# Kernel tuning notes

Hardware: AMD Instinct MI355X
Metric: run time of the kernel (lower is better)

## Reference

```python
import jax, jax.numpy as jnp
import numpy as np

N = 100000
E = 1600000
F_IN = 128
H = 128


def setup_inputs() -> dict:
    key = jax.random.key(0)
    ks = jax.random.split(key, 12)
    x = jax.random.normal(ks[0], (N, F_IN), dtype=jnp.float32)
    edge_index = jax.random.randint(ks[1], (2, E), 0, N, dtype=jnp.int64)
    s = 1.0 / np.sqrt(F_IN)
    sh = 1.0 / np.sqrt(H)
    inp = {"x": x, "edge_index": edge_index}
    # SAGEConv params: lin_l (neighbor agg, with bias), lin_r (root, no bias)
    inp["W1l"] = jax.random.uniform(ks[2], (H, F_IN), jnp.float32, -s, s)
    inp["b1"] = jnp.zeros((H,), jnp.float32)
    inp["W1r"] = jax.random.uniform(ks[3], (H, F_IN), jnp.float32, -s, s)
    inp["W2l"] = jax.random.uniform(ks[4], (H, H), jnp.float32, -sh, sh)
    inp["b2"] = jnp.zeros((H,), jnp.float32)
    inp["W2r"] = jax.random.uniform(ks[5], (H, H), jnp.float32, -sh, sh)
    inp["W3l"] = jax.random.uniform(ks[6], (H, H), jnp.float32, -sh, sh)
    inp["b3"] = jnp.zeros((H,), jnp.float32)
    inp["W3r"] = jax.random.uniform(ks[7], (H, H), jnp.float32, -sh, sh)
    inp["Wo"] = jax.random.uniform(ks[8], (1, H), jnp.float32, -sh, sh)
    inp["bo"] = jnp.zeros((1,), jnp.float32)
    return inp


def _sage_max(h, src, dst, Wl, bl, Wr):
    # max-aggregate source features at destination nodes (empty -> 0, as PyG)
    m = jax.ops.segment_max(h[src], dst, num_segments=N)  # [N, d]
    m = jnp.where(jnp.isfinite(m), m, jnp.zeros_like(m))
    return m @ Wl.T + bl + h @ Wr.T


def reference(x, edge_index, W1l, b1, W1r, W2l, b2, W2r, W3l, b3, W3r, Wo, bo):
    src, dst = edge_index[0], edge_index[1]
    h1 = jax.nn.elu(_sage_max(x, src, dst, W1l, b1, W1r))
    h2 = jax.nn.elu(_sage_max(h1, src, dst, W2l, b2, W2r)) + h1
    h3 = jax.nn.elu(_sage_max(h2, src, dst, W3l, b3, W3r)) + h2
    return jax.nn.sigmoid(h3 @ Wo.T + bo)  # [N, 1]
```

## Files before the change

kernel.cpp:

```cpp
#include <hip/hip_runtime.h>
#include <hip/hip_fp16.h>
#include <math.h>

#define HDIM 128

#define BSHIFT 7
#define BW 128
#define BCAP 4096
#define NBKMAX 1024
#define CHUNK 4096

typedef __attribute__((ext_vector_type(8))) _Float16 f16x8;
typedef __attribute__((ext_vector_type(2))) _Float16 f16x2;
typedef __attribute__((ext_vector_type(16))) float f32x16;
typedef unsigned int uint32;
typedef unsigned short u16;

__device__ __forceinline__ uint32 hmax2u(uint32 a, uint32 b) {
    f16x2 ha = __builtin_bit_cast(f16x2, a);
    f16x2 hb = __builtin_bit_cast(f16x2, b);
    f16x2 r = __builtin_elementwise_max(ha, hb);
    return __builtin_bit_cast(uint32, r);
}
__device__ __forceinline__ uint32 hadd2u(uint32 a, uint32 b) {
    f16x2 ha = __builtin_bit_cast(f16x2, a);
    f16x2 hb = __builtin_bit_cast(f16x2, b);
    f16x2 r = ha + hb;
    return __builtin_bit_cast(uint32, r);
}


__global__ __launch_bounds__(256) void bucket_bin(
    const int* __restrict__ ei, int E_, int nbk,
    int* __restrict__ bucketCnt, uint32* __restrict__ tmp)
{
    __shared__ int cnt[NBKMAX];
    __shared__ int gbase[NBKMAX];
    const int t = threadIdx.x;
    const int start = blockIdx.x * CHUNK;
    const int end = min(start + CHUNK, E_);

    for (int i = t; i < nbk; i += 256) cnt[i] = 0;
    __syncthreads();
    for (int e = start + t; e < end; e += 256)
        atomicAdd(&cnt[ei[E_ + e] >> BSHIFT], 1);
    __syncthreads();
    for (int i = t; i < nbk; i += 256) {
        int c = cnt[i];
        gbase[i] = c ? atomicAdd(&bucketCnt[i], c) : 0;
    }
    __syncthreads();
    for (int i = t; i < nbk; i += 256) cnt[i] = 0;
    __syncthreads();
    for (int e = start + t; e < end; e += 256) {
        int d = ei[E_ + e];
        int s = ei[e];
        int b = d >> BSHIFT;
        int r = atomicAdd(&cnt[b], 1);
        tmp[(size_t)b * BCAP + gbase[b] + r] =
            ((uint32)(d & (BW - 1)) << 17) | (uint32)s;
    }
}

__global__ __launch_bounds__(1024) void bucket_scan(
    const int* __restrict__ bucketCnt, int* __restrict__ bucketBase,
    int nbk, int* __restrict__ off, int N_, int E_) {
    __shared__ int sd[1024];
    int t = threadIdx.x;
    int v = (t < nbk) ? bucketCnt[t] : 0;
    sd[t] = v;
    __syncthreads();
    for (int ofs = 1; ofs < 1024; ofs <<= 1) {
        int add = (t >= ofs) ? sd[t - ofs] : 0;
        __syncthreads();
        sd[t] += add;
        __syncthreads();
    }
    if (t < nbk) bucketBase[t] = sd[t] - v;
    if (t == 0) off[N_] = E_;
}

__global__ __launch_bounds__(256) void bucket_csr(
    const uint32* __restrict__ tmp, const int* __restrict__ bucketCnt,
    const int* __restrict__ bucketBase,
    int* __restrict__ off, int* __restrict__ srcs, int N_)
{
    __shared__ int lc[BW];
    __shared__ int lo[BW];
    __shared__ int sd[256];
    const int b = blockIdx.x, t = threadIdx.x;
    const int cnt = bucketCnt[b], base = bucketBase[b];
    const uint32* tp = tmp + (size_t)b * BCAP;

    if (t < BW) lc[t] = 0;
    __syncthreads();
    for (int i = t; i < cnt; i += 256) atomicAdd(&lc[tp[i] >> 17], 1);
    __syncthreads();

    int v = (t < BW) ? lc[t] : 0;
    sd[t] = v;
    __syncthreads();
    for (int ofs = 1; ofs < 256; ofs <<= 1) {
        int add = (t >= ofs) ? sd[t - ofs] : 0;
        __syncthreads();
        sd[t] += add;
        __syncthreads();
    }
    if (t < BW) lo[t] = sd[t] - v;
    __syncthreads();

    for (int i = t; i < BW; i += 256) {
        int node = b * BW + i;
        if (node < N_) off[node] = base + lo[i];
    }
    if (t < BW) lc[t] = lo[t];
    __syncthreads();
    for (int i = t; i < cnt; i += 256) {
        uint32 p = tp[i];
        int dl = p >> 17, s = p & 0x1FFFF;
        int pos = base + atomicAdd(&lc[dl], 1);
        srcs[pos] = s;
    }
}


__global__ void cast_x(const float* __restrict__ x, uint32* __restrict__ xb, int n2) {
    int i = blockIdx.x * 256 + threadIdx.x;
    if (i >= n2) return;
    float2 v = ((const float2*)x)[i];
    f16x2 h = { (_Float16)v.x, (_Float16)v.y };
    xb[i] = __builtin_bit_cast(uint32, h);
}

__global__ void cast_weights_packed(
    const float* __restrict__ W1l, const float* __restrict__ W1r,
    const float* __restrict__ W2l, const float* __restrict__ W2r,
    const float* __restrict__ W3l, const float* __restrict__ W3r,
    f16x8* __restrict__ PW)
{
    int tid = blockIdx.x * 256 + threadIdx.x;
    if (tid >= 3 * 4096) return;
    int layer = tid >> 12, rem = tid & 4095;
    int g = rem >> 10, ks = (rem >> 6) & 15, lane = rem & 63;
    int col = g * 32 + (lane & 31), kq = lane >> 5;
    const float* src;
    if (layer == 0)      src = (ks < 8) ? W1l : W1r;
    else if (layer == 1) src = (ks < 8) ? W2l : W2r;
    else                 src = (ks < 8) ? W3l : W3r;
    int kk = (ks & 7) * 16 + kq * 8;
    f16x8 v;
#pragma unroll
    for (int j = 0; j < 8; ++j) v[j] = (_Float16)src[col * HDIM + kk + j];
    PW[tid] = v;
}


#define ESTRIDE 136
#define EDGE_CAP 832

#define RED16(m0,m1,m2,m3,V) do { \
    m0 = hmax2u(m0, (V)[0].x); m1 = hmax2u(m1, (V)[0].y); \
    m2 = hmax2u(m2, (V)[0].z); m3 = hmax2u(m3, (V)[0].w); \
    m0 = hmax2u(m0, (V)[1].x); m1 = hmax2u(m1, (V)[1].y); \
    m2 = hmax2u(m2, (V)[1].z); m3 = hmax2u(m3, (V)[1].w); \
    m0 = hmax2u(m0, (V)[2].x); m1 = hmax2u(m1, (V)[2].y); \
    m2 = hmax2u(m2, (V)[2].z); m3 = hmax2u(m3, (V)[2].w); \
    m0 = hmax2u(m0, (V)[3].x); m1 = hmax2u(m1, (V)[3].y); \
    m2 = hmax2u(m2, (V)[3].z); m3 = hmax2u(m3, (V)[3].w); \
} while (0)

template<bool L>
__device__ __forceinline__ void issue_batch(
    const uint4* __restrict__ hp, const int* __restrict__ srcs,
    const int* sedge, int estart, int eb, int e1, int es, int ch, uint4* v)
{
    int last = e1 - 1;
#pragma unroll
    for (int k = 0; k < 4; ++k) {
        int idx = min(eb + es + 4 * k, last);
        int s = L ? sedge[idx - estart] : srcs[idx];
        v[k] = hp[(size_t)s * 16 + ch];
    }
}

template<bool L>
__device__ __forceinline__ void gather8(
    const uint4* __restrict__ hp, const int* __restrict__ srcs,
    const int* sedge, int estart, int offv, int es, int ch, int w,
    uint4* sm)
{
    const uint32 NINF = 0xFC00FC00u;
    uint4 vb[2][4];

    int e0 = __shfl(offv, 0), e1 = __shfl(offv, 1);
    bool has = e1 > e0;
    if (has) issue_batch<L>(hp, srcs, sedge, estart, e0, e1, es, ch, vb[0]);

#pragma unroll
    for (int i = 0; i < 8; ++i) {
        int e0n = 0, e1n = 0; bool hasn = false;
        if (i + 1 < 8) {
            e0n = __shfl(offv, i + 1); e1n = __shfl(offv, i + 2);
            hasn = e1n > e0n;
            if (hasn) issue_batch<L>(hp, srcs, sedge, estart, e0n, e1n, es, ch, vb[(i + 1) & 1]);
        }
        uint32 m0 = NINF, m1 = NINF, m2 = NINF, m3 = NINF;
        if (has) {
            RED16(m0, m1, m2, m3, vb[i & 1]);
            for (int eb = e0 + 16; eb < e1; eb += 16) {
                issue_batch<L>(hp, srcs, sedge, estart, eb, e1, es, ch, vb[i & 1]);
                RED16(m0, m1, m2, m3, vb[i & 1]);
            }
        }
        m0 = hmax2u(m0, __shfl_xor(m0, 16)); m0 = hmax2u(m0, __shfl_xor(m0, 32));
        m1 = hmax2u(m1, __shfl_xor(m1, 16)); m1 = hmax2u(m1, __shfl_xor(m1, 32));
        m2 = hmax2u(m2, __shfl_xor(m2, 16)); m2 = hmax2u(m2, __shfl_xor(m2, 32));
        m3 = hmax2u(m3, __shfl_xor(m3, 16)); m3 = hmax2u(m3, __shfl_xor(m3, 32));
        if (es == 0) {
            int row = w * 8 + i;
            uint4 rr = make_uint4(0u, 0u, 0u, 0u);
            if (has) { rr.x = m0; rr.y = m1; rr.z = m2; rr.w = m3; }
            sm[row * 16 + (ch ^ (row & 7))] = rr;
        }
        e0 = e0n; e1 = e1n; has = hasn;
    }
}

__global__ __launch_bounds__(256, 8) void fused_layer(
    const uint32* __restrict__ hb,
    const int* __restrict__ off, const int* __restrict__ srcs,
    uint4* __restrict__ outb,
    const uint4* __restrict__ PW,
    const float* __restrict__ bias,
    int use_res,
    const float* __restrict__ Wo, const float* __restrict__ bo,
    float* __restrict__ out, int n_nodes)
{
    __shared__ alignas(16) char smemA[32 * ESTRIDE * 2];
    __shared__ uint4 sh[512];
    __shared__ int soff[33];
    __shared__ int sedge[EDGE_CAP];
    uint4*     sm = (uint4*)smemA;
    _Float16*  ho = (_Float16*)smemA;

    const int t = threadIdx.x, lane = t & 63, w = t >> 6;
    const int base = blockIdx.x * 32;
    const int l31 = lane & 31, kq = lane >> 5;
    const uint4* hp = (const uint4*)hb;

    if (t < 33) soff[t] = off[min(base + t, n_nodes)];

#pragma unroll
    for (int r = 0; r < 2; ++r) {
        int g = r * 256 + t;
        int row = g >> 4, c = g & 15;
        sh[row * 16 + (c ^ (row & 7))] = hp[(size_t)(base + row) * 16 + c];
    }

    const int estart = off[base];
    const int eend = off[min(base + 32, n_nodes)];
    const int ecnt = eend - estart;
    const bool useLds = (ecnt <= EDGE_CAP);
    const int scount = useLds ? ecnt : 0;
    for (int i = t; i < scount; i += 256) sedge[i] = srcs[estart + i];
    __syncthreads();

    const int es = lane >> 4, ch = lane & 15;
    const int offv = soff[w * 8 + min(lane, 8)];
    if (useLds) gather8<true >(hp, srcs, sedge, estart, offv, es, ch, w, sm);
    else        gather8<false>(hp, srcs, sedge, estart, offv, es, ch, w, sm);
    __syncthreads();

    f32x16 acc = {};
#pragma unroll
    for (int k = 0; k < 8; ++k) {
        f16x8 a = __builtin_bit_cast(f16x8, sm[l31 * 16 + ((2 * k + kq) ^ (l31 & 7))]);
        f16x8 b = __builtin_bit_cast(f16x8, PW[(w * 16 + k) * 64 + lane]);
        acc = __builtin_amdgcn_mfma_f32_32x32x16_f16(a, b, acc, 0, 0, 0);
    }
#pragma unroll
    for (int k = 0; k < 8; ++k) {
        f16x8 a = __builtin_bit_cast(f16x8, sh[l31 * 16 + ((2 * k + kq) ^ (l31 & 7))]);
        f16x8 b = __builtin_bit_cast(f16x8, PW[(w * 16 + 8 + k) * 64 + lane]);
        acc = __builtin_amdgcn_mfma_f32_32x32x16_f16(a, b, acc, 0, 0, 0);
    }

    __syncthreads();

    const int C = w * 32 + l31;
    const float bv = bias[C];
#pragma unroll
    for (int r = 0; r < 16; ++r) {
        int row = (r & 3) + 8 * (r >> 2) + 4 * kq;
        float v = acc[r] + bv;
        v = (v > 0.f) ? v : (__expf(v) - 1.f);
        ho[row * ESTRIDE + C] = (_Float16)v;
    }
    __syncthreads();

#pragma unroll
    for (int r = 0; r < 2; ++r) {
        int g = r * 256 + t;
        int row = g >> 4, c = g & 15;
        int R = base + row;
        bool valid = (R < n_nodes);
        uint4 v = *(const uint4*)&ho[row * ESTRIDE + c * 8];
        if (use_res) {
            uint4 rv = sh[row * 16 + (c ^ (row & 7))];
            v.x = hadd2u(v.x, rv.x); v.y = hadd2u(v.y, rv.y);
            v.z = hadd2u(v.z, rv.z); v.w = hadd2u(v.w, rv.w);
        }
        if (outb) {
            if (valid) outb[(size_t)R * 16 + c] = v;
        } else {
            const float* wo = Wo + c * 8;
            f16x2 a0 = __builtin_bit_cast(f16x2, v.x);
            f16x2 a1 = __builtin_bit_cast(f16x2, v.y);
            f16x2 a2 = __builtin_bit_cast(f16x2, v.z);
            f16x2 a3 = __builtin_bit_cast(f16x2, v.w);
            float s = (float)a0.x * wo[0] + (float)a0.y * wo[1]
                    + (float)a1.x * wo[2] + (float)a1.y * wo[3]
                    + (float)a2.x * wo[4] + (float)a2.y * wo[5]
                    + (float)a3.x * wo[6] + (float)a3.y * wo[7];
#pragma unroll
            for (int o = 8; o; o >>= 1) s += __shfl_down(s, o, 16);
            if (valid && (t & 15) == 0)
                out[R] = 1.f / (1.f + expf(-(s + bo[0])));
        }
    }
}


extern "C" void kernel_launch(void* const* d_in, const int* in_sizes, int n_in,
                              void* d_out, int out_size, void* d_ws, size_t ws_size,
                              hipStream_t stream) {
    const float* x   = (const float*)d_in[0];
    const int*   ei  = (const int*)d_in[1];
    const float* W1l = (const float*)d_in[2];
    const float* b1  = (const float*)d_in[3];
    const float* W1r = (const float*)d_in[4];
    const float* W2l = (const float*)d_in[5];
    const float* b2  = (const float*)d_in[6];
    const float* W2r = (const float*)d_in[7];
    const float* W3l = (const float*)d_in[8];
    const float* b3  = (const float*)d_in[9];
    const float* W3r = (const float*)d_in[10];
    const float* Wo  = (const float*)d_in[11];
    const float* bo  = (const float*)d_in[12];
    float* out = (float*)d_out;

    const int N_ = in_sizes[0] / HDIM;
    const int E_ = in_sizes[1] / 2;
    const int Np = (N_ + 127) & ~127;
    const int nbk = (N_ + BW - 1) / BW;

    size_t o = 0;
    auto carve = [&](size_t bytes) { size_t r = o; o = (o + bytes + 255) & ~255ULL; return r; };
    char* ws = (char*)d_ws;
    int* off        = (int*)(ws + carve((size_t)(N_ + 1) * 4));
    int* bucketCnt  = (int*)(ws + carve((size_t)NBKMAX * 4));
    int* bucketBase = (int*)(ws + carve((size_t)NBKMAX * 4));
    int* srcs       = (int*)(ws + carve((size_t)E_ * 4));
    uint32* tmp     = (uint32*)(ws + carve((size_t)nbk * BCAP * 4));
    uint4* PW       = (uint4*)(ws + carve((size_t)3 * 4096 * 16));
    uint32* XB      = (uint32*)(ws + carve((size_t)Np * 64 * 4));
    uint32* H1B     = (uint32*)(ws + carve((size_t)Np * 64 * 4));
    (void)ws_size; (void)n_in; (void)out_size;

    (void)hipMemsetAsync(bucketCnt, 0, (size_t)NBKMAX * 4, stream);
    bucket_bin<<<(E_ + CHUNK - 1) / CHUNK, 256, 0, stream>>>(ei, E_, nbk, bucketCnt, tmp);
    bucket_scan<<<1, 1024, 0, stream>>>(bucketCnt, bucketBase, nbk, off, N_, E_);
    bucket_csr<<<nbk, 256, 0, stream>>>(tmp, bucketCnt, bucketBase, off, srcs, N_);

    cast_weights_packed<<<(3 * 4096 + 255) / 256, 256, 0, stream>>>(
        W1l, W1r, W2l, W2r, W3l, W3r, (f16x8*)PW);
    cast_x<<<(N_ * 64 + 255) / 256, 256, 0, stream>>>(x, XB, N_ * 64);

    const int nbF = (N_ + 31) / 32;

    const uint4* PW1 = PW;
    const uint4* PW2 = PW + 4096;
    const uint4* PW3 = PW + 8192;

    fused_layer<<<nbF, 256, 0, stream>>>(XB, off, srcs, (uint4*)H1B, PW1, b1,
                                         0, nullptr, nullptr, nullptr, N_);
    fused_layer<<<nbF, 256, 0, stream>>>(H1B, off, srcs, (uint4*)XB, PW2, b2,
                                         1, nullptr, nullptr, nullptr, N_);
    fused_layer<<<nbF, 256, 0, stream>>>(XB, off, srcs, nullptr, PW3, b3,
                                         1, Wo, bo, out, N_);
}
```

Measured before the change: 368.3 us.

## Coarsely sort CSR neighbor lists by source range and relax launch bounds

```diff
diff --git a/kernel.cpp b/kernel.cpp
--- a/kernel.cpp
+++ b/kernel.cpp
@@ -9,6 +9,7 @@
 #define BCAP 4096
 #define NBKMAX 1024
 #define CHUNK 4096
+#define SBINS 16
 
 typedef __attribute__((ext_vector_type(8))) _Float16 f16x8;
 typedef __attribute__((ext_vector_type(2))) _Float16 f16x2;
@@ -85,20 +86,25 @@
     const int* __restrict__ bucketBase,
     int* __restrict__ off, int* __restrict__ srcs, int N_)
 {
-    __shared__ int lc[BW];
-    __shared__ int lo[BW];
+    __shared__ int lo[BW * SBINS];
     __shared__ int sd[256];
     const int b = blockIdx.x, t = threadIdx.x;
     const int cnt = bucketCnt[b], base = bucketBase[b];
     const uint32* tp = tmp + (size_t)b * BCAP;
 
-    if (t < BW) lc[t] = 0;
-    __syncthreads();
-    for (int i = t; i < cnt; i += 256) atomicAdd(&lc[tp[i] >> 17], 1);
-    __syncthreads();
-
-    int v = (t < BW) ? lc[t] : 0;
-    sd[t] = v;
+    for (int i = t; i < BW * SBINS; i += 256) lo[i] = 0;
+    __syncthreads();
+    for (int i = t; i < cnt; i += 256) {
+        uint32 p = tp[i];
+        int key = (int)(p >> 17) * SBINS + (int)((p & 0x1FFFF) >> 13);
+        atomicAdd(&lo[key], 1);
+    }
+    __syncthreads();
+
+    int loc[8], s = 0;
+#pragma unroll
+    for (int k = 0; k < 8; ++k) { loc[k] = s; s += lo[8 * t + k]; }
+    sd[t] = s;
     __syncthreads();
     for (int ofs = 1; ofs < 256; ofs <<= 1) {
         int add = (t >= ofs) ? sd[t - ofs] : 0;
@@ -106,20 +112,23 @@
         sd[t] += add;
         __syncthreads();
     }
-    if (t < BW) lo[t] = sd[t] - v;
+    const int tb = sd[t] - s;
+#pragma unroll
+    for (int k = 0; k < 8; ++k) lo[8 * t + k] = tb + loc[k];
     __syncthreads();
 
     for (int i = t; i < BW; i += 256) {
         int node = b * BW + i;
-        if (node < N_) off[node] = base + lo[i];
-    }
-    if (t < BW) lc[t] = lo[t];
-    __syncthreads();
+        if (node < N_) off[node] = base + lo[i * SBINS];
+    }
+    __syncthreads();
+
     for (int i = t; i < cnt; i += 256) {
         uint32 p = tp[i];
-        int dl = p >> 17, s = p & 0x1FFFF;
-        int pos = base + atomicAdd(&lc[dl], 1);
-        srcs[pos] = s;
+        int src = (int)(p & 0x1FFFF);
+        int key = (int)(p >> 17) * SBINS + (src >> 13);
+        int pos = base + atomicAdd(&lo[key], 1);
+        srcs[pos] = src;
     }
 }
 
@@ -226,7 +235,7 @@
     }
 }
 
-__global__ __launch_bounds__(256, 8) void fused_layer(
+__global__ __launch_bounds__(256, 6) void fused_layer(
     const uint32* __restrict__ hb,
     const int* __restrict__ off, const int* __restrict__ srcs,
     uint4* __restrict__ outb,
```

Result: faster. 357.0 us (-3.1%).

## Replace bucketed CSR build with global-atomic histogram, scan, scatter; merge prep kernels

Applied to the files above, without the earlier changes.

```diff
diff --git a/kernel.cpp b/kernel.cpp
--- a/kernel.cpp
+++ b/kernel.cpp
@@ -3,12 +3,6 @@
 #include <math.h>
 
 #define HDIM 128
-
-#define BSHIFT 7
-#define BW 128
-#define BCAP 4096
-#define NBKMAX 1024
-#define CHUNK 4096
 
 typedef __attribute__((ext_vector_type(8))) _Float16 f16x8;
 typedef __attribute__((ext_vector_type(2))) _Float16 f16x2;
@@ -30,45 +24,54 @@
 }
 
 
-__global__ __launch_bounds__(256) void bucket_bin(
-    const int* __restrict__ ei, int E_, int nbk,
-    int* __restrict__ bucketCnt, uint32* __restrict__ tmp)
-{
-    __shared__ int cnt[NBKMAX];
-    __shared__ int gbase[NBKMAX];
+__global__ __launch_bounds__(256) void prep(
+    const float* __restrict__ x, const int* __restrict__ ei,
+    const float* __restrict__ W1l, const float* __restrict__ W1r,
+    const float* __restrict__ W2l, const float* __restrict__ W2r,
+    const float* __restrict__ W3l, const float* __restrict__ W3r,
+    f16x8* __restrict__ PW, uint32* __restrict__ xb,
+    int* __restrict__ off,
+    int E_, int N_, int nbW, int nbX)
+{
+    const int bid = blockIdx.x, t = threadIdx.x;
+    if (bid < nbW) {
+        int tid = bid * 256 + t;
+        if (tid >= 3 * 4096) return;
+        int layer = tid >> 12, rem = tid & 4095;
+        int g = rem >> 10, ks = (rem >> 6) & 15, lane = rem & 63;
+        int col = g * 32 + (lane & 31), kq = lane >> 5;
+        const float* src;
+        if (layer == 0)      src = (ks < 8) ? W1l : W1r;
+        else if (layer == 1) src = (ks < 8) ? W2l : W2r;
+        else                 src = (ks < 8) ? W3l : W3r;
+        int kk = (ks & 7) * 16 + kq * 8;
+        f16x8 v;
+#pragma unroll
+        for (int j = 0; j < 8; ++j) v[j] = (_Float16)src[col * HDIM + kk + j];
+        PW[tid] = v;
+    } else if (bid < nbW + nbX) {
+        int i = (bid - nbW) * 256 + t;
+        if (i >= N_ * 64) return;
+        float2 v = ((const float2*)x)[i];
+        f16x2 h = { (_Float16)v.x, (_Float16)v.y };
+        xb[i] = __builtin_bit_cast(uint32, h);
+    } else {
+        int e = (bid - nbW - nbX) * 256 + t;
+        if (e < E_) atomicAdd(&off[ei[E_ + e] + 1], 1);
+    }
+}
+
+
+__global__ __launch_bounds__(1024) void scan_off(
+    int* __restrict__ off, int* __restrict__ cur, int N_)
+{
+    __shared__ int sd[1024];
     const int t = threadIdx.x;
-    const int start = blockIdx.x * CHUNK;
-    const int end = min(start + CHUNK, E_);
-
-    for (int i = t; i < nbk; i += 256) cnt[i] = 0;
-    __syncthreads();
-    for (int e = start + t; e < end; e += 256)
-        atomicAdd(&cnt[ei[E_ + e] >> BSHIFT], 1);
-    __syncthreads();
-    for (int i = t; i < nbk; i += 256) {
-        int c = cnt[i];
-        gbase[i] = c ? atomicAdd(&bucketCnt[i], c) : 0;
-    }
-    __syncthreads();
-    for (int i = t; i < nbk; i += 256) cnt[i] = 0;
-    __syncthreads();
-    for (int e = start + t; e < end; e += 256) {
-        int d = ei[E_ + e];
-        int s = ei[e];
-        int b = d >> BSHIFT;
-        int r = atomicAdd(&cnt[b], 1);
-        tmp[(size_t)b * BCAP + gbase[b] + r] =
-            ((uint32)(d & (BW - 1)) << 17) | (uint32)s;
-    }
-}
-
-__global__ __launch_bounds__(1024) void bucket_scan(
-    const int* __restrict__ bucketCnt, int* __restrict__ bucketBase,
-    int nbk, int* __restrict__ off, int N_, int E_) {
-    __shared__ int sd[1024];
-    int t = threadIdx.x;
-    int v = (t < nbk) ? bucketCnt[t] : 0;
-    sd[t] = v;
+    const int CH = (N_ + 1 + 1023) >> 10;
+    const int lo = t * CH, hi = min(lo + CH, N_ + 1);
+    int s = 0;
+    for (int i = lo; i < hi; ++i) s += off[i];
+    sd[t] = s;
     __syncthreads();
     for (int ofs = 1; ofs < 1024; ofs <<= 1) {
         int add = (t >= ofs) ? sd[t - ofs] : 0;
@@ -76,82 +79,23 @@
         sd[t] += add;
         __syncthreads();
     }
-    if (t < nbk) bucketBase[t] = sd[t] - v;
-    if (t == 0) off[N_] = E_;
-}
-
-__global__ __launch_bounds__(256) void bucket_csr(
-    const uint32* __restrict__ tmp, const int* __restrict__ bucketCnt,
-    const int* __restrict__ bucketBase,
-    int* __restrict__ off, int* __restrict__ srcs, int N_)
-{
-    __shared__ int lc[BW];
-    __shared__ int lo[BW];
-    __shared__ int sd[256];
-    const int b = blockIdx.x, t = threadIdx.x;
-    const int cnt = bucketCnt[b], base = bucketBase[b];
-    const uint32* tp = tmp + (size_t)b * BCAP;
-
-    if (t < BW) lc[t] = 0;
-    __syncthreads();
-    for (int i = t; i < cnt; i += 256) atomicAdd(&lc[tp[i] >> 17], 1);
-    __syncthreads();
-
-    int v = (t < BW) ? lc[t] : 0;
-    sd[t] = v;
-    __syncthreads();
-    for (int ofs = 1; ofs < 256; ofs <<= 1) {
-        int add = (t >= ofs) ? sd[t - ofs] : 0;
-        __syncthreads();
-        sd[t] += add;
-        __syncthreads();
-    }
-    if (t < BW) lo[t] = sd[t] - v;
-    __syncthreads();
-
-    for (int i = t; i < BW; i += 256) {
-        int node = b * BW + i;
-        if (node < N_) off[node] = base + lo[i];
-    }
-    if (t < BW) lc[t] = lo[t];
-    __syncthreads();
-    for (int i = t; i < cnt; i += 256) {
-        uint32 p = tp[i];
-        int dl = p >> 17, s = p & 0x1FFFF;
-        int pos = base + atomicAdd(&lc[dl], 1);
-        srcs[pos] = s;
-    }
-}
-
-
-__global__ void cast_x(const float* __restrict__ x, uint32* __restrict__ xb, int n2) {
-    int i = blockIdx.x * 256 + threadIdx.x;
-    if (i >= n2) return;
-    float2 v = ((const float2*)x)[i];
-    f16x2 h = { (_Float16)v.x, (_Float16)v.y };
-    xb[i] = __builtin_bit_cast(uint32, h);
-}
-
-__global__ void cast_weights_packed(
-    const float* __restrict__ W1l, const float* __restrict__ W1r,
-    const float* __restrict__ W2l, const float* __restrict__ W2r,
-    const float* __restrict__ W3l, const float* __restrict__ W3r,
-    f16x8* __restrict__ PW)
-{
-    int tid = blockIdx.x * 256 + threadIdx.x;
-    if (tid >= 3 * 4096) return;
-    int layer = tid >> 12, rem = tid & 4095;
-    int g = rem >> 10, ks = (rem >> 6) & 15, lane = rem & 63;
-    int col = g * 32 + (lane & 31), kq = lane >> 5;
-    const float* src;
-    if (layer == 0)      src = (ks < 8) ? W1l : W1r;
-    else if (layer == 1) src = (ks < 8) ? W2l : W2r;
-    else                 src = (ks < 8) ? W3l : W3r;
-    int kk = (ks & 7) * 16 + kq * 8;
-    f16x8 v;
-#pragma unroll
-    for (int j = 0; j < 8; ++j) v[j] = (_Float16)src[col * HDIM + kk + j];
-    PW[tid] = v;
+    int run = sd[t] - s;
+    for (int i = lo; i < hi; ++i) {
+        run += off[i];
+        off[i] = run;
+        if (i < N_) cur[i] = run;
+    }
+}
+
+
+__global__ __launch_bounds__(256) void scatter_edges(
+    const int* __restrict__ ei, int* __restrict__ cur,
+    int* __restrict__ srcs, int E_)
+{
+    int e = blockIdx.x * 256 + threadIdx.x;
+    if (e >= E_) return;
+    int s = ei[e], d = ei[E_ + e];
+    srcs[atomicAdd(&cur[d], 1)] = s;
 }
 
 
@@ -226,7 +170,7 @@
     }
 }
 
-__global__ __launch_bounds__(256, 8) void fused_layer(
+__global__ __launch_bounds__(256, 6) void fused_layer(
     const uint32* __restrict__ hb,
     const int* __restrict__ off, const int* __restrict__ srcs,
     uint4* __restrict__ outb,
@@ -352,29 +296,26 @@
     const int N_ = in_sizes[0] / HDIM;
     const int E_ = in_sizes[1] / 2;
     const int Np = (N_ + 127) & ~127;
-    const int nbk = (N_ + BW - 1) / BW;
 
     size_t o = 0;
     auto carve = [&](size_t bytes) { size_t r = o; o = (o + bytes + 255) & ~255ULL; return r; };
     char* ws = (char*)d_ws;
     int* off        = (int*)(ws + carve((size_t)(N_ + 1) * 4));
-    int* bucketCnt  = (int*)(ws + carve((size_t)NBKMAX * 4));
-    int* bucketBase = (int*)(ws + carve((size_t)NBKMAX * 4));
+    int* cur        = (int*)(ws + carve((size_t)N_ * 4));
     int* srcs       = (int*)(ws + carve((size_t)E_ * 4));
-    uint32* tmp     = (uint32*)(ws + carve((size_t)nbk * BCAP * 4));
     uint4* PW       = (uint4*)(ws + carve((size_t)3 * 4096 * 16));
     uint32* XB      = (uint32*)(ws + carve((size_t)Np * 64 * 4));
     uint32* H1B     = (uint32*)(ws + carve((size_t)Np * 64 * 4));
     (void)ws_size; (void)n_in; (void)out_size;
 
-    (void)hipMemsetAsync(bucketCnt, 0, (size_t)NBKMAX * 4, stream);
-    bucket_bin<<<(E_ + CHUNK - 1) / CHUNK, 256, 0, stream>>>(ei, E_, nbk, bucketCnt, tmp);
-    bucket_scan<<<1, 1024, 0, stream>>>(bucketCnt, bucketBase, nbk, off, N_, E_);
-    bucket_csr<<<nbk, 256, 0, stream>>>(tmp, bucketCnt, bucketBase, off, srcs, N_);
-
-    cast_weights_packed<<<(3 * 4096 + 255) / 256, 256, 0, stream>>>(
-        W1l, W1r, W2l, W2r, W3l, W3r, (f16x8*)PW);
-    cast_x<<<(N_ * 64 + 255) / 256, 256, 0, stream>>>(x, XB, N_ * 64);
+    (void)hipMemsetAsync(off, 0, (size_t)(N_ + 1) * 4, stream);
+    const int nbW = (3 * 4096 + 255) / 256;
+    const int nbX = (N_ * 64 + 255) / 256;
+    const int nbH = (E_ + 255) / 256;
+    prep<<<nbW + nbX + nbH, 256, 0, stream>>>(
+        x, ei, W1l, W1r, W2l, W2r, W3l, W3r, (f16x8*)PW, XB, off, E_, N_, nbW, nbX);
+    scan_off<<<1, 1024, 0, stream>>>(off, cur, N_);
+    scatter_edges<<<nbH, 256, 0, stream>>>(ei, cur, srcs, E_);
 
     const int nbF = (N_ + 31) / 32;
 
```

After: 704.1 us. 1.91x slower.

## Merge preprocessing kernels into one launch and fold bucket scan into CSR build

Applied to the files above, without the earlier changes.

```diff
diff --git a/kernel.cpp b/kernel.cpp
--- a/kernel.cpp
+++ b/kernel.cpp
@@ -30,66 +30,100 @@
 }
 
 
-__global__ __launch_bounds__(256) void bucket_bin(
-    const int* __restrict__ ei, int E_, int nbk,
-    int* __restrict__ bucketCnt, uint32* __restrict__ tmp)
+__global__ __launch_bounds__(256) void prep(
+    const float* __restrict__ x, const int* __restrict__ ei,
+    const float* __restrict__ W1l, const float* __restrict__ W1r,
+    const float* __restrict__ W2l, const float* __restrict__ W2r,
+    const float* __restrict__ W3l, const float* __restrict__ W3r,
+    f16x8* __restrict__ PW, uint32* __restrict__ xb,
+    int* __restrict__ bucketCnt, uint32* __restrict__ tmp,
+    int E_, int N_, int nbk, int nbW, int nbX)
 {
     __shared__ int cnt[NBKMAX];
     __shared__ int gbase[NBKMAX];
-    const int t = threadIdx.x;
-    const int start = blockIdx.x * CHUNK;
-    const int end = min(start + CHUNK, E_);
-
-    for (int i = t; i < nbk; i += 256) cnt[i] = 0;
-    __syncthreads();
-    for (int e = start + t; e < end; e += 256)
-        atomicAdd(&cnt[ei[E_ + e] >> BSHIFT], 1);
-    __syncthreads();
-    for (int i = t; i < nbk; i += 256) {
-        int c = cnt[i];
-        gbase[i] = c ? atomicAdd(&bucketCnt[i], c) : 0;
-    }
-    __syncthreads();
-    for (int i = t; i < nbk; i += 256) cnt[i] = 0;
-    __syncthreads();
-    for (int e = start + t; e < end; e += 256) {
-        int d = ei[E_ + e];
-        int s = ei[e];
-        int b = d >> BSHIFT;
-        int r = atomicAdd(&cnt[b], 1);
-        tmp[(size_t)b * BCAP + gbase[b] + r] =
-            ((uint32)(d & (BW - 1)) << 17) | (uint32)s;
-    }
-}
-
-__global__ __launch_bounds__(1024) void bucket_scan(
-    const int* __restrict__ bucketCnt, int* __restrict__ bucketBase,
-    int nbk, int* __restrict__ off, int N_, int E_) {
-    __shared__ int sd[1024];
-    int t = threadIdx.x;
-    int v = (t < nbk) ? bucketCnt[t] : 0;
-    sd[t] = v;
-    __syncthreads();
-    for (int ofs = 1; ofs < 1024; ofs <<= 1) {
-        int add = (t >= ofs) ? sd[t - ofs] : 0;
-        __syncthreads();
-        sd[t] += add;
-        __syncthreads();
-    }
-    if (t < nbk) bucketBase[t] = sd[t] - v;
-    if (t == 0) off[N_] = E_;
-}
+    const int bid = blockIdx.x, t = threadIdx.x;
+
+    if (bid < nbW) {
+        int tid = bid * 256 + t;
+        if (tid >= 3 * 4096) return;
+        int layer = tid >> 12, rem = tid & 4095;
+        int g = rem >> 10, ks = (rem >> 6) & 15, lane = rem & 63;
+        int col = g * 32 + (lane & 31), kq = lane >> 5;
+        const float* src;
+        if (layer == 0)      src = (ks < 8) ? W1l : W1r;
+        else if (layer == 1) src = (ks < 8) ? W2l : W2r;
+        else                 src = (ks < 8) ? W3l : W3r;
+        int kk = (ks & 7) * 16 + kq * 8;
+        f16x8 v;
+#pragma unroll
+        for (int j = 0; j < 8; ++j) v[j] = (_Float16)src[col * HDIM + kk + j];
+        PW[tid] = v;
+    } else if (bid < nbW + nbX) {
+        int i = (bid - nbW) * 256 + t;
+        if (i >= N_ * 64) return;
+        float2 v = ((const float2*)x)[i];
+        f16x2 h = { (_Float16)v.x, (_Float16)v.y };
+        xb[i] = __builtin_bit_cast(uint32, h);
+    } else {
+        const int start = (bid - nbW - nbX) * CHUNK;
+        const int end = min(start + CHUNK, E_);
+        for (int i = t; i < nbk; i += 256) cnt[i] = 0;
+        __syncthreads();
+        for (int e = start + t; e < end; e += 256)
+            atomicAdd(&cnt[ei[E_ + e] >> BSHIFT], 1);
+        __syncthreads();
+        for (int i = t; i < nbk; i += 256) {
+            int c = cnt[i];
+            gbase[i] = c ? atomicAdd(&bucketCnt[i], c) : 0;
+        }
+        __syncthreads();
+        for (int i = t; i < nbk; i += 256) cnt[i] = 0;
+        __syncthreads();
+        for (int e = start + t; e < end; e += 256) {
+            int d = ei[E_ + e];
+            int s = ei[e];
+            int b = d >> BSHIFT;
+            int r = atomicAdd(&cnt[b], 1);
+            tmp[(size_t)b * BCAP + gbase[b] + r] =
+                ((uint32)(d & (BW - 1)) << 17) | (uint32)s;
+        }
+    }
+}
+
 
 __global__ __launch_bounds__(256) void bucket_csr(
     const uint32* __restrict__ tmp, const int* __restrict__ bucketCnt,
-    const int* __restrict__ bucketBase,
-    int* __restrict__ off, int* __restrict__ srcs, int N_)
+    int* __restrict__ off, int* __restrict__ srcs, int N_, int E_, int nbk)
 {
     __shared__ int lc[BW];
     __shared__ int lo[BW];
     __shared__ int sd[256];
+    __shared__ int sbase;
     const int b = blockIdx.x, t = threadIdx.x;
-    const int cnt = bucketCnt[b], base = bucketBase[b];
+
+    int p = 0;
+#pragma unroll
+    for (int k = 0; k < 4; ++k) {
+        int i = 4 * t + k;
+        p += (i < nbk) ? bucketCnt[i] : 0;
+    }
+    sd[t] = p;
+    __syncthreads();
+    for (int ofs = 1; ofs < 256; ofs <<= 1) {
+        int add = (t >= ofs) ? sd[t - ofs] : 0;
+        __syncthreads();
+        sd[t] += add;
+        __syncthreads();
+    }
+    if (t == 0) {
+        int c = b >> 2;
+        int base = c ? sd[c - 1] : 0;
+        for (int i = 4 * c; i < b; ++i) base += bucketCnt[i];
+        sbase = base;
+        if (b == 0) off[N_] = E_;
+    }
+    __syncthreads();
+    const int base = sbase, cnt = bucketCnt[b];
     const uint32* tp = tmp + (size_t)b * BCAP;
 
     if (t < BW) lc[t] = 0;
@@ -116,42 +150,11 @@
     if (t < BW) lc[t] = lo[t];
     __syncthreads();
     for (int i = t; i < cnt; i += 256) {
-        uint32 p = tp[i];
-        int dl = p >> 17, s = p & 0x1FFFF;
+        uint32 p2 = tp[i];
+        int dl = p2 >> 17, s = p2 & 0x1FFFF;
         int pos = base + atomicAdd(&lc[dl], 1);
         srcs[pos] = s;
     }
-}
-
-
-__global__ void cast_x(const float* __restrict__ x, uint32* __restrict__ xb, int n2) {
-    int i = blockIdx.x * 256 + threadIdx.x;
-    if (i >= n2) return;
-    float2 v = ((const float2*)x)[i];
-    f16x2 h = { (_Float16)v.x, (_Float16)v.y };
-    xb[i] = __builtin_bit_cast(uint32, h);
-}
-
-__global__ void cast_weights_packed(
-    const float* __restrict__ W1l, const float* __restrict__ W1r,
-    const float* __restrict__ W2l, const float* __restrict__ W2r,
-    const float* __restrict__ W3l, const float* __restrict__ W3r,
-    f16x8* __restrict__ PW)
-{
-    int tid = blockIdx.x * 256 + threadIdx.x;
-    if (tid >= 3 * 4096) return;
-    int layer = tid >> 12, rem = tid & 4095;
-    int g = rem >> 10, ks = (rem >> 6) & 15, lane = rem & 63;
-    int col = g * 32 + (lane & 31), kq = lane >> 5;
-    const float* src;
-    if (layer == 0)      src = (ks < 8) ? W1l : W1r;
-    else if (layer == 1) src = (ks < 8) ? W2l : W2r;
-    else                 src = (ks < 8) ? W3l : W3r;
-    int kk = (ks & 7) * 16 + kq * 8;
-    f16x8 v;
-#pragma unroll
-    for (int j = 0; j < 8; ++j) v[j] = (_Float16)src[col * HDIM + kk + j];
-    PW[tid] = v;
 }
 
 
@@ -226,7 +229,7 @@
     }
 }
 
-__global__ __launch_bounds__(256, 8) void fused_layer(
+__global__ __launch_bounds__(256, 6) void fused_layer(
     const uint32* __restrict__ hb,
     const int* __restrict__ off, const int* __restrict__ srcs,
     uint4* __restrict__ outb,
@@ -359,7 +362,6 @@
     char* ws = (char*)d_ws;
     int* off        = (int*)(ws + carve((size_t)(N_ + 1) * 4));
     int* bucketCnt  = (int*)(ws + carve((size_t)NBKMAX * 4));
-    int* bucketBase = (int*)(ws + carve((size_t)NBKMAX * 4));
     int* srcs       = (int*)(ws + carve((size_t)E_ * 4));
     uint32* tmp     = (uint32*)(ws + carve((size_t)nbk * BCAP * 4));
     uint4* PW       = (uint4*)(ws + carve((size_t)3 * 4096 * 16));
@@ -368,13 +370,15 @@
     (void)ws_size; (void)n_in; (void)out_size;
 
     (void)hipMemsetAsync(bucketCnt, 0, (size_t)NBKMAX * 4, stream);
-    bucket_bin<<<(E_ + CHUNK - 1) / CHUNK, 256, 0, stream>>>(ei, E_, nbk, bucketCnt, tmp);
-    bucket_scan<<<1, 1024, 0, stream>>>(bucketCnt, bucketBase, nbk, off, N_, E_);
-    bucket_csr<<<nbk, 256, 0, stream>>>(tmp, bucketCnt, bucketBase, off, srcs, N_);
-
-    cast_weights_packed<<<(3 * 4096 + 255) / 256, 256, 0, stream>>>(
-        W1l, W1r, W2l, W2r, W3l, W3r, (f16x8*)PW);
-    cast_x<<<(N_ * 64 + 255) / 256, 256, 0, stream>>>(x, XB, N_ * 64);
+
+    const int nbW = (3 * 4096 + 255) / 256;
+    const int nbX = (N_ * 64 + 255) / 256;
+    const int nbB = (E_ + CHUNK - 1) / CHUNK;
+    prep<<<nbW + nbX + nbB, 256, 0, stream>>>(
+        x, ei, W1l, W1r, W2l, W2r, W3l, W3r,
+        (f16x8*)PW, XB, bucketCnt, tmp, E_, N_, nbk, nbW, nbX);
+
+    bucket_csr<<<nbk, 256, 0, stream>>>(tmp, bucketCnt, off, srcs, N_, E_, nbk);
 
     const int nbF = (N_ + 31) / 32;
 
```

New measurement: 368.5 us. About the same (+0.1%).
